# Kernel tuning notes

Hardware: AMD Instinct MI355X
Metric: run time of the kernel (lower is better)

Reference implementation:

```python
import jax, jax.numpy as jnp
import numpy as np

BS, SLEN = 4, 4096
H, ZD, VD = 8, 128, 256
CHUNK = 1024
NEG = -1e9


def _rope(x, cos, sin):
    # x: [B, S, H, D]; cos/sin: [S, D//2] (llama-style complex pair rotation)
    b, s, h, d = x.shape
    xr, xi = x.reshape(b, s, h, d // 2, 2)[..., 0], x.reshape(b, s, h, d // 2, 2)[..., 1]
    c = cos[None, :, None, :]
    sn = sin[None, :, None, :]
    orr = xr * c - xi * sn
    oii = xr * sn + xi * c
    return jnp.stack([orr, oii], axis=-1).reshape(b, s, h, d)


def setup_inputs() -> dict:
    key = jax.random.key(0)
    k1, k2, k3 = jax.random.split(key, 3)
    xq = jax.random.normal(k1, (BS, SLEN, H * ZD), dtype=jnp.float32)
    xk = jax.random.normal(k2, (BS, SLEN, H * ZD), dtype=jnp.float32)
    xv = jax.random.normal(k3, (BS, SLEN, H * VD), dtype=jnp.float32)
    # rotary tables over one chunk
    freqs = 1.0 / (10000.0 ** (np.arange(0, ZD, 2, dtype=np.float32) / ZD))  # [ZD//2]
    t = np.arange(CHUNK, dtype=np.float32)
    ang = np.outer(t, freqs)  # [CHUNK, ZD//2]
    cos = jnp.asarray(np.cos(ang), dtype=jnp.float32)
    sin = jnp.asarray(np.sin(ang), dtype=jnp.float32)
    # additive causal mask within a chunk
    causal = np.tril(np.ones((CHUNK, CHUNK), dtype=bool))
    mask = jnp.asarray(np.where(causal, 0.0, NEG).astype(np.float32))
    return {"xq": xq, "xk": xk, "xv": xv, "mask": mask, "cos": cos, "sin": sin}


def reference(xq, xk, xv, mask, cos, sin):
    bs, slen, _ = xq.shape
    nc = slen // CHUNK
    q = xq.reshape(bs * nc, CHUNK, H, ZD)
    k = xk.reshape(bs * nc, CHUNK, H, ZD)
    v = xv.reshape(bs * nc, CHUNK, H, VD)
    # RoPE applied after chunking (slen > chunk_size path)
    q = _rope(q, cos, sin)
    k = _rope(k, cos, sin)
    # block-local causal attention, no 1/sqrt(d) scaling (faithful to source)
    scores = jnp.einsum("bqhd,bkhd->bhqk", q, k) + mask[None, None, :, :]
    probs = jax.nn.softmax(scores.astype(jnp.float32), axis=-1).astype(q.dtype)
    out = jnp.einsum("bhqk,bkhd->bqhd", probs, v)
    return out.reshape(bs, slen, H * VD)
```

## Files before the change

### kernel.cpp

```cpp
#include <hip/hip_runtime.h>


#define NHEAD 8
#define ZDIM  128
#define VDIM  256
#define CHUNK 1024
#define QTILE 128
#define KT    32
#define NW    4

typedef _Float16 f16x8 __attribute__((ext_vector_type(8)));
typedef _Float16 f16x4 __attribute__((ext_vector_type(4)));
typedef __fp16   h16x2 __attribute__((ext_vector_type(2)));
typedef float    f32x4  __attribute__((ext_vector_type(4)));
typedef float    f32x16 __attribute__((ext_vector_type(16)));
typedef unsigned int u32;

#define KSTRIDE 128
#define VSTRIDE 36
#define LOG2E   1.44269504088896f
#define RTHR    11.5415603f

__global__ __launch_bounds__(256, 2)
void attn_fused(const float* __restrict__ xq, const float* __restrict__ xk,
                const float* __restrict__ xv, const float* __restrict__ cosT,
                const float* __restrict__ sinT, float* __restrict__ out)
{
  __shared__ _Float16 Klds[2][KT * KSTRIDE];
  __shared__ _Float16 Vlds[2][VDIM * VSTRIDE];

  const int b = (int)blockIdx.x;
  const int d = (b & 7) * 64 + (b >> 3);
  const int qpair = d & 3;
  const int ch = d >> 2;
  const int h  = ch & 7;
  const int cb = ch >> 3;

  const int tid  = threadIdx.x;
  const int w    = tid >> 6;
  const int lane = tid & 63;
  const int l31  = lane & 31;
  const int hi   = lane >> 5;
  const int vswz = (l31 >> 3) & 3;
  const int kswz = l31 & 7;

  const size_t row0 = (size_t)cb * CHUNK;

  const int kr    = tid >> 3;
  const int kt8   = tid & 7;
  const int vg    = tid >> 5;
  const int vc0   = (tid & 31) * 8;
  const int vsw   = tid & 3;
  const int vflip = ((tid >> 2) & 1) * 4;
  const int kblk  = vg >> 1;
  const int inb   = (vg & 1) * 4;

  int buf = 0;

  for (int half = 0; half < 2; ++half) {
    const int qt = half ? qpair : (7 - qpair);
    const int wq0 = qt * QTILE + w * 32;
    const int qg  = wq0 + l31;

    f16x8 qfrag[8];
    {
      const float* qp = xq + (row0 + qg) * (size_t)(NHEAD * ZDIM) + h * ZDIM;
      const float* cq = cosT + qg * (ZDIM / 2);
      const float* sq = sinT + qg * (ZDIM / 2);
#pragma unroll
      for (int dblk = 0; dblk < 8; ++dblk) {
        const int d0 = dblk * 16 + hi * 8;
        f32x4 a  = *(const f32x4*)(qp + d0);
        f32x4 b2 = *(const f32x4*)(qp + d0 + 4);
        f32x4 cv = *(const f32x4*)(cq + (d0 >> 1));
        f32x4 sv = *(const f32x4*)(sq + (d0 >> 1));
        union { h16x2 h2[4]; f16x8 v; } fr;
#pragma unroll
        for (int p = 0; p < 4; ++p) {
          const float xr = (p < 2 ? a[2 * p] : b2[2 * p - 4]);
          const float xi = (p < 2 ? a[2 * p + 1] : b2[2 * p - 3]);
          fr.h2[p] = __builtin_amdgcn_cvt_pkrtz((xr * cv[p] - xi * sv[p]) * LOG2E,
                                                (xr * sv[p] + xi * cv[p]) * LOG2E);
        }
        qfrag[dblk] = fr.v;
      }
    }

    const f32x16 zf = {};
    f32x16 acc[8];
#pragma unroll
    for (int g = 0; g < 8; ++g) acc[g] = zf;
    float mrun = -1e30f;
    float lrun = 0.f;

    const int nkt = 4 * (qt + 1);

    for (int kt = 0; kt < nkt; ++kt) {
      const int ktb = kt * KT;
      {
        const int krow = ktb + kr;
        const float* kpb = xk + (row0 + krow) * (size_t)(NHEAD * ZDIM) + h * ZDIM;
        const float* ckb = cosT + krow * (ZDIM / 2);
        const float* skb = sinT + krow * (ZDIM / 2);
        f32x4 a0 = *(const f32x4*)(kpb + 8 * kt8);
        f32x4 a1 = *(const f32x4*)(kpb + 8 * kt8 + 4);
        f32x4 ca = *(const f32x4*)(ckb + 4 * kt8);
        f32x4 sa = *(const f32x4*)(skb + 4 * kt8);
        f32x4 b0 = *(const f32x4*)(kpb + 8 * kt8 + 64);
        f32x4 b1 = *(const f32x4*)(kpb + 8 * kt8 + 68);
        f32x4 cbv = *(const f32x4*)(ckb + 4 * kt8 + 32);
        f32x4 sbv = *(const f32x4*)(skb + 4 * kt8 + 32);
        union { h16x2 h2[4]; f16x8 v; } koA, koB;
#pragma unroll
        for (int p = 0; p < 4; ++p) {
          const float xrA = (p < 2 ? a0[2 * p] : a1[2 * p - 4]);
          const float xiA = (p < 2 ? a0[2 * p + 1] : a1[2 * p - 3]);
          koA.h2[p] = __builtin_amdgcn_cvt_pkrtz(xrA * ca[p] - xiA * sa[p],
                                                 xrA * sa[p] + xiA * ca[p]);
          const float xrB = (p < 2 ? b0[2 * p] : b1[2 * p - 4]);
          const float xiB = (p < 2 ? b0[2 * p + 1] : b1[2 * p - 3]);
          koB.h2[p] = __builtin_amdgcn_cvt_pkrtz(xrB * cbv[p] - xiB * sbv[p],
                                                 xrB * sbv[p] + xiB * cbv[p]);
        }
        const int sw = kr & 7;
        *(f16x8*)&Klds[buf][kr * KSTRIDE + ((kt8 ^ sw) * 8)]       = koA.v;
        *(f16x8*)&Klds[buf][kr * KSTRIDE + (((kt8 + 8) ^ sw) * 8)] = koB.v;
      }
      {
        const int vrow = ktb + vg * 4;
        const float* vp = xv + (row0 + vrow) * (size_t)(NHEAD * VDIM) + h * VDIM + vc0;
        f32x4 v0 = *(const f32x4*)(vp);         f32x4 v1 = *(const f32x4*)(vp + 4);
        f32x4 v2 = *(const f32x4*)(vp + 2048);  f32x4 v3 = *(const f32x4*)(vp + 2052);
        f32x4 v4 = *(const f32x4*)(vp + 4096);  f32x4 v5 = *(const f32x4*)(vp + 4100);
        f32x4 v6 = *(const f32x4*)(vp + 6144);  f32x4 v7 = *(const f32x4*)(vp + 6148);
#pragma unroll
        for (int ci = 0; ci < 8; ++ci) {
          const float e0 = (ci < 4 ? v0[ci] : v1[ci - 4]);
          const float e1 = (ci < 4 ? v2[ci] : v3[ci - 4]);
          const float e2 = (ci < 4 ? v4[ci] : v5[ci - 4]);
          const float e3 = (ci < 4 ? v6[ci] : v7[ci - 4]);
          union { h16x2 a2[2]; f16x4 v; } t;
          t.a2[0] = __builtin_amdgcn_cvt_pkrtz(e0, e1);
          t.a2[1] = __builtin_amdgcn_cvt_pkrtz(e2, e3);
          *(f16x4*)&Vlds[buf][(vc0 + ci) * VSTRIDE + ((kblk ^ vsw) * 8) + (inb ^ vflip)] = t.v;
        }
      }
      __syncthreads();

      if (ktb <= wq0 + 31) {
        f32x16 s = {};
        __builtin_amdgcn_s_setprio(1);
#pragma unroll
        for (int dblk = 0; dblk < 8; ++dblk) {
          f16x8 kf = *(const f16x8*)&Klds[buf][l31 * KSTRIDE + (((dblk * 2 + hi) ^ kswz) * 8)];
          s = __builtin_amdgcn_mfma_f32_32x32x16_f16(kf, qfrag[dblk], s, 0, 0, 0);
        }
        __builtin_amdgcn_s_setprio(0);

        if (ktb + 31 > wq0) {
#pragma unroll
          for (int r = 0; r < 16; ++r) {
            const int kg = ktb + ((r & 3) + 8 * (r >> 2) + 4 * hi);
            if (kg > qg) s[r] = -1.0e9f;
          }
        }

        float m = s[0];
#pragma unroll
        for (int r = 1; r < 16; ++r) m = fmaxf(m, s[r]);
        m = fmaxf(m, __shfl_xor(m, 32));
        const bool need = (m > mrun + RTHR);
        if (__any(need)) {
          const float Mn = fmaxf(mrun, m);
          const float al = exp2f(mrun - Mn);
          mrun = Mn;
          lrun *= al;
#pragma unroll
          for (int r = 0; r < 16; ++r) {
            const float alr = __shfl(al, (r & 3) + 8 * (r >> 2) + 4 * hi);
#pragma unroll
            for (int g = 0; g < 8; ++g) acc[g][r] *= alr;
          }
        }
        float pr[16];
        float lsum = 0.f;
#pragma unroll
        for (int r = 0; r < 16; ++r) {
          pr[r] = exp2f(s[r] - mrun);
          lsum += pr[r];
        }
        lrun += lsum;

#pragma unroll
        for (int kb = 0; kb < 2; ++kb) {
          union { h16x2 h; u32 u; } A_, B_, C_, D_;
          A_.h = __builtin_amdgcn_cvt_pkrtz(pr[8 * kb + 0], pr[8 * kb + 1]);
          B_.h = __builtin_amdgcn_cvt_pkrtz(pr[8 * kb + 2], pr[8 * kb + 3]);
          C_.h = __builtin_amdgcn_cvt_pkrtz(pr[8 * kb + 4], pr[8 * kb + 5]);
          D_.h = __builtin_amdgcn_cvt_pkrtz(pr[8 * kb + 6], pr[8 * kb + 7]);
          const u32 G1 = hi ? A_.u : C_.u;
          const u32 G2 = hi ? B_.u : D_.u;
          const u32 G1s = (u32)__shfl_xor((int)G1, 32);
          const u32 G2s = (u32)__shfl_xor((int)G2, 32);
          union { u32 u[4]; f16x8 v; } af;
          af.u[0] = hi ? G1s : A_.u;
          af.u[1] = hi ? G2s : B_.u;
          af.u[2] = hi ? C_.u : G1s;
          af.u[3] = hi ? D_.u : G2s;
          __builtin_amdgcn_s_setprio(1);
#pragma unroll
          for (int g = 0; g < 8; ++g) {
            const int vcol = g * 32 + l31;
            const int ck = (((kb * 2 + hi) ^ vswz) * 8);
            const int fl = (g & 1) * 4;
            union { f16x4 h4[2]; f16x8 v; } bf;
            bf.h4[0] = *(const f16x4*)&Vlds[buf][vcol * VSTRIDE + ck + fl];
            bf.h4[1] = *(const f16x4*)&Vlds[buf][vcol * VSTRIDE + ck + (fl ^ 4)];
            acc[g] = __builtin_amdgcn_mfma_f32_32x32x16_f16(af.v, bf.v, acc[g], 0, 0, 0);
          }
          __builtin_amdgcn_s_setprio(0);
        }
      }
      buf ^= 1;
    }

    const float ls = lrun + __shfl_xor(lrun, 32);
    const float linv = 1.0f / ls;
#pragma unroll
    for (int r = 0; r < 16; ++r) {
      const int qloc = (r & 3) + 8 * (r >> 2) + 4 * hi;
      const float lr = __shfl(linv, qloc);
      const size_t ob = (row0 + wq0 + qloc) * (size_t)(NHEAD * VDIM) + h * VDIM + l31;
#pragma unroll
      for (int g = 0; g < 8; ++g)
        out[ob + g * 32] = acc[g][r] * lr;
    }
    __syncthreads();
  }
}

extern "C" void kernel_launch(void* const* d_in, const int* in_sizes, int n_in,
                              void* d_out, int out_size, void* d_ws, size_t ws_size,
                              hipStream_t stream) {
  const float* xq   = (const float*)d_in[0];
  const float* xk   = (const float*)d_in[1];
  const float* xv   = (const float*)d_in[2];
  const float* cosT = (const float*)d_in[4];
  const float* sinT = (const float*)d_in[5];
  float* out = (float*)d_out;

  dim3 grid(512);
  dim3 block(256);
  attn_fused<<<grid, block, 0, stream>>>(xq, xk, xv, cosT, sinT, out);
}
```

Before: 182.0 us.

## Prefetch next K/V tile into registers during compute of current tile

```diff
diff --git a/kernel.cpp b/kernel.cpp
--- a/kernel.cpp
+++ b/kernel.cpp
@@ -57,16 +57,74 @@
 
   int buf = 0;
 
+  f32x4 pk0, pk1, pk2, pk3;
+  f32x4 pv0, pv1, pv2, pv3, pv4, pv5, pv6, pv7;
+
+#define LOADT(ktb_)                                                       \
+  do {                                                                    \
+    const int krow_ = (ktb_) + kr;                                        \
+    const float* kpb_ = xk + (row0 + krow_) * (size_t)(NHEAD * ZDIM) + h * ZDIM; \
+    pk0 = *(const f32x4*)(kpb_ + 8 * kt8);                                \
+    pk1 = *(const f32x4*)(kpb_ + 8 * kt8 + 4);                            \
+    pk2 = *(const f32x4*)(kpb_ + 8 * kt8 + 64);                           \
+    pk3 = *(const f32x4*)(kpb_ + 8 * kt8 + 68);                           \
+    const int vrow_ = (ktb_) + vg * 4;                                    \
+    const float* vp_ = xv + (row0 + vrow_) * (size_t)(NHEAD * VDIM) + h * VDIM + vc0; \
+    pv0 = *(const f32x4*)(vp_);         pv1 = *(const f32x4*)(vp_ + 4);   \
+    pv2 = *(const f32x4*)(vp_ + 2048);  pv3 = *(const f32x4*)(vp_ + 2052);\
+    pv4 = *(const f32x4*)(vp_ + 4096);  pv5 = *(const f32x4*)(vp_ + 4100);\
+    pv6 = *(const f32x4*)(vp_ + 6144);  pv7 = *(const f32x4*)(vp_ + 6148);\
+  } while (0)
+
+#define WRITET(ktb_)                                                      \
+  do {                                                                    \
+    const int krow_ = (ktb_) + kr;                                        \
+    const float* ckb_ = cosT + krow_ * (ZDIM / 2);                        \
+    const float* skb_ = sinT + krow_ * (ZDIM / 2);                        \
+    f32x4 ca  = *(const f32x4*)(ckb_ + 4 * kt8);                          \
+    f32x4 sa  = *(const f32x4*)(skb_ + 4 * kt8);                          \
+    f32x4 cbv = *(const f32x4*)(ckb_ + 4 * kt8 + 32);                     \
+    f32x4 sbv = *(const f32x4*)(skb_ + 4 * kt8 + 32);                     \
+    union { h16x2 h2[4]; f16x8 v; } koA, koB;                             \
+    _Pragma("unroll")                                                     \
+    for (int p = 0; p < 4; ++p) {                                         \
+      const float xrA = (p < 2 ? pk0[2 * p] : pk1[2 * p - 4]);            \
+      const float xiA = (p < 2 ? pk0[2 * p + 1] : pk1[2 * p - 3]);        \
+      koA.h2[p] = __builtin_amdgcn_cvt_pkrtz(xrA * ca[p] - xiA * sa[p],   \
+                                             xrA * sa[p] + xiA * ca[p]);  \
+      const float xrB = (p < 2 ? pk2[2 * p] : pk3[2 * p - 4]);            \
+      const float xiB = (p < 2 ? pk2[2 * p + 1] : pk3[2 * p - 3]);        \
+      koB.h2[p] = __builtin_amdgcn_cvt_pkrtz(xrB * cbv[p] - xiB * sbv[p], \
+                                             xrB * sbv[p] + xiB * cbv[p]);\
+    }                                                                     \
+    const int sw_ = kr & 7;                                               \
+    *(f16x8*)&Klds[buf][kr * KSTRIDE + ((kt8 ^ sw_) * 8)]       = koA.v;  \
+    *(f16x8*)&Klds[buf][kr * KSTRIDE + (((kt8 + 8) ^ sw_) * 8)] = koB.v;  \
+    _Pragma("unroll")                                                     \
+    for (int ci = 0; ci < 8; ++ci) {                                      \
+      const float e0 = (ci < 4 ? pv0[ci] : pv1[ci - 4]);                  \
+      const float e1 = (ci < 4 ? pv2[ci] : pv3[ci - 4]);                  \
+      const float e2 = (ci < 4 ? pv4[ci] : pv5[ci - 4]);                  \
+      const float e3 = (ci < 4 ? pv6[ci] : pv7[ci - 4]);                  \
+      union { h16x2 a2[2]; f16x4 v; } t;                                  \
+      t.a2[0] = __builtin_amdgcn_cvt_pkrtz(e0, e1);                       \
+      t.a2[1] = __builtin_amdgcn_cvt_pkrtz(e2, e3);                       \
+      *(f16x4*)&Vlds[buf][(vc0 + ci) * VSTRIDE + ((kblk ^ vsw) * 8) + (inb ^ vflip)] = t.v; \
+    }                                                                     \
+  } while (0)
+
   for (int half = 0; half < 2; ++half) {
     const int qt = half ? qpair : (7 - qpair);
     const int wq0 = qt * QTILE + w * 32;
-    const int qg  = wq0 + l31;
+    const int qgr = wq0 + l31;
+
+    LOADT(0);
 
     f16x8 qfrag[8];
     {
-      const float* qp = xq + (row0 + qg) * (size_t)(NHEAD * ZDIM) + h * ZDIM;
-      const float* cq = cosT + qg * (ZDIM / 2);
-      const float* sq = sinT + qg * (ZDIM / 2);
+      const float* qp = xq + (row0 + qgr) * (size_t)(NHEAD * ZDIM) + h * ZDIM;
+      const float* cq = cosT + qgr * (ZDIM / 2);
+      const float* sq = sinT + qgr * (ZDIM / 2);
 #pragma unroll
       for (int dblk = 0; dblk < 8; ++dblk) {
         const int d0 = dblk * 16 + hi * 8;
@@ -97,54 +155,9 @@
 
     for (int kt = 0; kt < nkt; ++kt) {
       const int ktb = kt * KT;
-      {
-        const int krow = ktb + kr;
-        const float* kpb = xk + (row0 + krow) * (size_t)(NHEAD * ZDIM) + h * ZDIM;
-        const float* ckb = cosT + krow * (ZDIM / 2);
-        const float* skb = sinT + krow * (ZDIM / 2);
-        f32x4 a0 = *(const f32x4*)(kpb + 8 * kt8);
-        f32x4 a1 = *(const f32x4*)(kpb + 8 * kt8 + 4);
-        f32x4 ca = *(const f32x4*)(ckb + 4 * kt8);
-        f32x4 sa = *(const f32x4*)(skb + 4 * kt8);
-        f32x4 b0 = *(const f32x4*)(kpb + 8 * kt8 + 64);
-        f32x4 b1 = *(const f32x4*)(kpb + 8 * kt8 + 68);
-        f32x4 cbv = *(const f32x4*)(ckb + 4 * kt8 + 32);
-        f32x4 sbv = *(const f32x4*)(skb + 4 * kt8 + 32);
-        union { h16x2 h2[4]; f16x8 v; } koA, koB;
-#pragma unroll
-        for (int p = 0; p < 4; ++p) {
-          const float xrA = (p < 2 ? a0[2 * p] : a1[2 * p - 4]);
-          const float xiA = (p < 2 ? a0[2 * p + 1] : a1[2 * p - 3]);
-          koA.h2[p] = __builtin_amdgcn_cvt_pkrtz(xrA * ca[p] - xiA * sa[p],
-                                                 xrA * sa[p] + xiA * ca[p]);
-          const float xrB = (p < 2 ? b0[2 * p] : b1[2 * p - 4]);
-          const float xiB = (p < 2 ? b0[2 * p + 1] : b1[2 * p - 3]);
-          koB.h2[p] = __builtin_amdgcn_cvt_pkrtz(xrB * cbv[p] - xiB * sbv[p],
-                                                 xrB * sbv[p] + xiB * cbv[p]);
-        }
-        const int sw = kr & 7;
-        *(f16x8*)&Klds[buf][kr * KSTRIDE + ((kt8 ^ sw) * 8)]       = koA.v;
-        *(f16x8*)&Klds[buf][kr * KSTRIDE + (((kt8 + 8) ^ sw) * 8)] = koB.v;
-      }
-      {
-        const int vrow = ktb + vg * 4;
-        const float* vp = xv + (row0 + vrow) * (size_t)(NHEAD * VDIM) + h * VDIM + vc0;
-        f32x4 v0 = *(const f32x4*)(vp);         f32x4 v1 = *(const f32x4*)(vp + 4);
-        f32x4 v2 = *(const f32x4*)(vp + 2048);  f32x4 v3 = *(const f32x4*)(vp + 2052);
-        f32x4 v4 = *(const f32x4*)(vp + 4096);  f32x4 v5 = *(const f32x4*)(vp + 4100);
-        f32x4 v6 = *(const f32x4*)(vp + 6144);  f32x4 v7 = *(const f32x4*)(vp + 6148);
-#pragma unroll
-        for (int ci = 0; ci < 8; ++ci) {
-          const float e0 = (ci < 4 ? v0[ci] : v1[ci - 4]);
-          const float e1 = (ci < 4 ? v2[ci] : v3[ci - 4]);
-          const float e2 = (ci < 4 ? v4[ci] : v5[ci - 4]);
-          const float e3 = (ci < 4 ? v6[ci] : v7[ci - 4]);
-          union { h16x2 a2[2]; f16x4 v; } t;
-          t.a2[0] = __builtin_amdgcn_cvt_pkrtz(e0, e1);
-          t.a2[1] = __builtin_amdgcn_cvt_pkrtz(e2, e3);
-          *(f16x4*)&Vlds[buf][(vc0 + ci) * VSTRIDE + ((kblk ^ vsw) * 8) + (inb ^ vflip)] = t.v;
-        }
-      }
+
+      WRITET(ktb);
+      if (kt + 1 < nkt) LOADT(ktb + KT);
       __syncthreads();
 
       if (ktb <= wq0 + 31) {
@@ -161,7 +174,7 @@
 #pragma unroll
           for (int r = 0; r < 16; ++r) {
             const int kg = ktb + ((r & 3) + 8 * (r >> 2) + 4 * hi);
-            if (kg > qg) s[r] = -1.0e9f;
+            if (kg > qgr) s[r] = -1.0e9f;
           }
         }
 
@@ -182,22 +195,21 @@
             for (int g = 0; g < 8; ++g) acc[g][r] *= alr;
           }
         }
-        float pr[16];
         float lsum = 0.f;
 #pragma unroll
         for (int r = 0; r < 16; ++r) {
-          pr[r] = exp2f(s[r] - mrun);
-          lsum += pr[r];
+          s[r] = exp2f(s[r] - mrun);
+          lsum += s[r];
         }
         lrun += lsum;
 
 #pragma unroll
         for (int kb = 0; kb < 2; ++kb) {
           union { h16x2 h; u32 u; } A_, B_, C_, D_;
-          A_.h = __builtin_amdgcn_cvt_pkrtz(pr[8 * kb + 0], pr[8 * kb + 1]);
-          B_.h = __builtin_amdgcn_cvt_pkrtz(pr[8 * kb + 2], pr[8 * kb + 3]);
-          C_.h = __builtin_amdgcn_cvt_pkrtz(pr[8 * kb + 4], pr[8 * kb + 5]);
-          D_.h = __builtin_amdgcn_cvt_pkrtz(pr[8 * kb + 6], pr[8 * kb + 7]);
+          A_.h = __builtin_amdgcn_cvt_pkrtz(s[8 * kb + 0], s[8 * kb + 1]);
+          B_.h = __builtin_amdgcn_cvt_pkrtz(s[8 * kb + 2], s[8 * kb + 3]);
+          C_.h = __builtin_amdgcn_cvt_pkrtz(s[8 * kb + 4], s[8 * kb + 5]);
+          D_.h = __builtin_amdgcn_cvt_pkrtz(s[8 * kb + 6], s[8 * kb + 7]);
           const u32 G1 = hi ? A_.u : C_.u;
           const u32 G2 = hi ? B_.u : D_.u;
           const u32 G1s = (u32)__shfl_xor((int)G1, 32);
@@ -237,6 +249,8 @@
     }
     __syncthreads();
   }
+#undef LOADT
+#undef WRITET
 }
 
 extern "C" void kernel_launch(void* const* d_in, const int* in_sizes, int n_in,
```

After: 268.6 us. 1.48x slower.
